# Performance work log

Measured on AMD Instinct MI355X. Metric: run time of the kernel, lower is better.

The kernel has to match this reference:

```python
import jax, jax.numpy as jnp
import numpy as np

D_MODEL = 768
N_HEAD = 12
D_K = D_MODEL // N_HEAD  # 64, also d_v
B, S = 2, 2048


def setup_inputs() -> dict:
    key = jax.random.key(0)
    ks = jax.random.split(key, 8)
    scale = 1.0 / np.sqrt(D_MODEL)
    return {
        "q": jax.random.normal(ks[0], (B, S, D_MODEL), dtype=jnp.float32),
        "k": jax.random.normal(ks[1], (B, S, D_MODEL), dtype=jnp.float32),
        "v": jax.random.normal(ks[2], (B, S, D_MODEL), dtype=jnp.float32),
        "mask": jax.random.randint(ks[3], (B, 1, S, S), 0, 2, dtype=jnp.int32),
        # per-head projection weights, stacked over heads: [H, d_model, d_k]
        "Wq": jax.random.normal(ks[4], (N_HEAD, D_MODEL, D_K), dtype=jnp.float32) * scale,
        "Wk": jax.random.normal(ks[5], (N_HEAD, D_MODEL, D_K), dtype=jnp.float32) * scale,
        "Wv": jax.random.normal(ks[6], (N_HEAD, D_MODEL, D_K), dtype=jnp.float32) * scale,
        # output projection: [n_head*d_v, d_model]
        "Wo": jax.random.normal(ks[7], (N_HEAD * D_K, D_MODEL), dtype=jnp.float32) * scale,
    }


def reference(q, k, v, mask, Wq, Wk, Wv, Wo):
    # Per-head projections (batched over heads instead of a python loop)
    qh = jnp.einsum("bsd,hdk->bhsk", q, Wq)  # [B,H,S,d_k]
    kh = jnp.einsum("bsd,hdk->bhsk", k, Wk)
    vh = jnp.einsum("bsd,hdk->bhsk", v, Wv)
    # Scaled dot-product attention with full score matrix (faithful to source)
    scores = jnp.einsum("bhsk,bhtk->bhst", qh, kh) / jnp.sqrt(jnp.asarray(D_K, qh.dtype))
    scores = jnp.where(mask == 0, jnp.asarray(-1e9, scores.dtype), scores)
    attn = jax.nn.softmax(scores, axis=-1)  # [B,H,S,S]
    out = jnp.einsum("bhst,bhtk->bhsk", attn, vh)  # [B,H,S,d_k]
    # concat heads (matches torch.cat over head outputs along last dim)
    out = out.transpose(0, 2, 1, 3).reshape(out.shape[0], out.shape[2], -1)  # [B,S,H*d_k]
    return out @ Wo  # [B,S,d_model]
```

## Files before the change

kernel.cpp:

```cpp
#include <hip/hip_runtime.h>
#include <stdint.h>

#define S_LEN 2048
#define NH 12
#define DM 768
#define DK 64
#define NB 2
#define MROWS (NB * S_LEN)

typedef __attribute__((ext_vector_type(8))) short short8;
typedef __attribute__((ext_vector_type(4))) float f32x4;
typedef __attribute__((ext_vector_type(4))) uint32_t u32x4;

__device__ __forceinline__ unsigned short bf16rne(float f) {
    union { float f; uint32_t u; } v; v.f = f;
    return (unsigned short)((v.u + 0x7FFFu + ((v.u >> 16) & 1u)) >> 16);
}

__device__ __forceinline__ uint32_t cvtpk(float lo, float hi) {
    uint32_t r;
    asm("v_cvt_pk_bf16_f32 %0, %1, %2" : "=v"(r) : "v"(lo), "v"(hi));
    return r;
}

__global__ __launch_bounds__(256) void prep_kernel(
        const float* __restrict__ Wq, const float* __restrict__ Wk,
        const float* __restrict__ Wv, const float* __restrict__ Wo,
        const int* __restrict__ mask,
        unsigned short* __restrict__ WqT, unsigned short* __restrict__ WkT,
        unsigned short* __restrict__ WvT, unsigned short* __restrict__ WoT,
        uint32_t* __restrict__ pm) {
    int bx = blockIdx.x;
    if (bx < 9216) {
        int which = bx / 2304;
        const float* W = (which == 0) ? Wq : (which == 1) ? Wk : (which == 2) ? Wv : Wo;
        unsigned short* WT = (which == 0) ? WqT : (which == 1) ? WkT : (which == 2) ? WvT : WoT;
        int idx = (bx % 2304) * 256 + threadIdx.x;
        int n = idx / DM, kd = idx % DM;
        float val;
        if (which < 3) { int h = n >> 6, kk = n & 63; val = W[(h * DM + kd) * DK + kk]; }
        else          { val = W[kd * DM + n]; }
        WT[idx] = bf16rne(val);
    } else {
        int t = (bx - 9216) * 256 + threadIdx.x;
        const int4* mp = (const int4*)mask;
        int4 a = mp[2 * t], b = mp[2 * t + 1];
        unsigned int by =
            (a.x != 0 ? 1u : 0u)  | (a.y != 0 ? 2u : 0u)  | (a.z != 0 ? 4u : 0u)  | (a.w != 0 ? 8u : 0u) |
            (b.x != 0 ? 16u : 0u) | (b.y != 0 ? 32u : 0u) | (b.z != 0 ? 64u : 0u) | (b.w != 0 ? 128u : 0u);
        ((unsigned char*)pm)[t] = (unsigned char)by;
    }
}

__device__ __forceinline__ void gemm_core(const unsigned short* __restrict__ A,
                                          const unsigned short* __restrict__ BT,
                                          unsigned short* As, unsigned short* Bs,
                                          f32x4 (&acc)[4][4]) {
    const int tid = threadIdx.x;
    const int lane = tid & 63, wid = tid >> 6;
    const int ww = wid & 1, wh = wid >> 1;
    const int quad = lane >> 4, l16 = lane & 15;
    const int lr = lane >> 2;
    const int lc = (lane & 3) * 8;
    typedef __attribute__((address_space(1))) const unsigned int* gp1;
    typedef __attribute__((address_space(3))) unsigned int* lp3;
    const unsigned short* Ag = A + (size_t)(wid * 32 + lr) * DM + lc;
    const unsigned short* Bg = BT + (size_t)(wid * 32 + lr) * DM + lc;
    unsigned short* Al = &As[wid * 32 * 32];
    unsigned short* Bl = &Bs[wid * 32 * 32];
    for (int kt = 0; kt < DM; kt += 32) {
        __syncthreads();
        __builtin_amdgcn_global_load_lds((gp1)(const void*)(Ag + kt),            (lp3)(void*)Al,             16, 0, 0);
        __builtin_amdgcn_global_load_lds((gp1)(const void*)(Ag + 16 * DM + kt),  (lp3)(void*)(Al + 16 * 32), 16, 0, 0);
        __builtin_amdgcn_global_load_lds((gp1)(const void*)(Bg + kt),            (lp3)(void*)Bl,             16, 0, 0);
        __builtin_amdgcn_global_load_lds((gp1)(const void*)(Bg + 16 * DM + kt),  (lp3)(void*)(Bl + 16 * 32), 16, 0, 0);
        __syncthreads();
        short8 af[4], bf[4];
#pragma unroll
        for (int i = 0; i < 4; ++i) af[i] = *(const short8*)&As[(wh * 64 + i * 16 + l16) * 32 + quad * 8];
#pragma unroll
        for (int j = 0; j < 4; ++j) bf[j] = *(const short8*)&Bs[(ww * 64 + j * 16 + l16) * 32 + quad * 8];
#pragma unroll
        for (int i = 0; i < 4; ++i)
#pragma unroll
            for (int j = 0; j < 4; ++j)
                acc[i][j] = __builtin_amdgcn_mfma_f32_16x16x32_bf16(af[i], bf[j], acc[i][j], 0, 0, 0);
    }
}

__device__ __forceinline__ void gemm_core_f32A(const float* __restrict__ A,
                                               const unsigned short* __restrict__ BT,
                                               unsigned short* As, unsigned short* Bs,
                                               f32x4 (&acc)[4][4]) {
    const int tid = threadIdx.x;
    const int lane = tid & 63, wid = tid >> 6;
    const int ww = wid & 1, wh = wid >> 1;
    const int quad = lane >> 4, l16 = lane & 15;
    const int lr = lane >> 2;
    const int lc = (lane & 3) * 8;
    typedef __attribute__((address_space(1))) const unsigned int* gp1;
    typedef __attribute__((address_space(3))) unsigned int* lp3;
    const float* Ag0 = A + (size_t)(wid * 32 + lr) * DM + lc;
    const float* Ag1 = A + (size_t)(wid * 32 + 16 + lr) * DM + lc;
    const unsigned short* Bg = BT + (size_t)(wid * 32 + lr) * DM + lc;
    unsigned short* Al = &As[wid * 32 * 32];
    unsigned short* Bl = &Bs[wid * 32 * 32];
    for (int kt = 0; kt < DM; kt += 32) {
        __syncthreads();
        __builtin_amdgcn_global_load_lds((gp1)(const void*)(Bg + kt),            (lp3)(void*)Bl,             16, 0, 0);
        __builtin_amdgcn_global_load_lds((gp1)(const void*)(Bg + 16 * DM + kt),  (lp3)(void*)(Bl + 16 * 32), 16, 0, 0);
        float4 x0 = *(const float4*)(Ag0 + kt), x1 = *(const float4*)(Ag0 + kt + 4);
        float4 y0 = *(const float4*)(Ag1 + kt), y1 = *(const float4*)(Ag1 + kt + 4);
        u32x4 ua, ub;
        ua[0] = cvtpk(x0.x, x0.y); ua[1] = cvtpk(x0.z, x0.w);
        ua[2] = cvtpk(x1.x, x1.y); ua[3] = cvtpk(x1.z, x1.w);
        ub[0] = cvtpk(y0.x, y0.y); ub[1] = cvtpk(y0.z, y0.w);
        ub[2] = cvtpk(y1.x, y1.y); ub[3] = cvtpk(y1.z, y1.w);
        *(u32x4*)&Al[lr * 32 + lc] = ua;
        *(u32x4*)&Al[(16 + lr) * 32 + lc] = ub;
        __syncthreads();
        short8 af[4], bf[4];
#pragma unroll
        for (int i = 0; i < 4; ++i) af[i] = *(const short8*)&As[(wh * 64 + i * 16 + l16) * 32 + quad * 8];
#pragma unroll
        for (int j = 0; j < 4; ++j) bf[j] = *(const short8*)&Bs[(ww * 64 + j * 16 + l16) * 32 + quad * 8];
#pragma unroll
        for (int i = 0; i < 4; ++i)
#pragma unroll
            for (int j = 0; j < 4; ++j)
                acc[i][j] = __builtin_amdgcn_mfma_f32_16x16x32_bf16(af[i], bf[j], acc[i][j], 0, 0, 0);
    }
}

__global__ __launch_bounds__(256) void proj_gemm(
        const float* __restrict__ qf32, const float* __restrict__ kf32,
        const float* __restrict__ vf32,
        const unsigned short* __restrict__ WqT, const unsigned short* __restrict__ WkT,
        const unsigned short* __restrict__ WvT,
        unsigned short* __restrict__ qh, unsigned short* __restrict__ kh,
        unsigned short* __restrict__ vhT) {
    __shared__ __align__(16) unsigned short As[128 * 32];
    __shared__ __align__(16) unsigned short Bs[128 * 32];
    const int z = blockIdx.z;
    const float* A = (z == 0) ? qf32 : (z == 1) ? kf32 : vf32;
    const unsigned short* BT = (z == 0) ? WqT : (z == 1) ? WkT : WvT;
    f32x4 acc[4][4] = {};
    gemm_core_f32A(A + (size_t)blockIdx.x * 128 * DM, BT + (size_t)blockIdx.y * 128 * DM, As, Bs, acc);

    const int tid = threadIdx.x;
    const int lane = tid & 63, wid = tid >> 6;
    const int ww = wid & 1, wh = wid >> 1;
    const int quad = lane >> 4, l16 = lane & 15;
    const int row0 = blockIdx.x * 128 + wh * 64;
    const int col0 = blockIdx.y * 128 + ww * 64;
    if (z < 2) {
        unsigned short* C = z ? kh : qh;
#pragma unroll
        for (int i = 0; i < 4; ++i)
#pragma unroll
            for (int j = 0; j < 4; ++j)
#pragma unroll
                for (int r = 0; r < 4; ++r)
                    C[(size_t)(row0 + i * 16 + quad * 4 + r) * DM + col0 + j * 16 + l16] = bf16rne(acc[i][j][r]);
    } else {
#pragma unroll
        for (int i = 0; i < 4; ++i)
#pragma unroll
            for (int j = 0; j < 4; ++j) {
                int row = row0 + i * 16 + quad * 4;
                int col = col0 + j * 16 + l16;
                int bb = row >> 11, s = row & 2047;
                int hh = col >> 6, d = col & 63;
                int g = (s >> 2) & 15;
                int pg = (g & 8) | ((g & 3) << 1) | ((g & 4) >> 2);
                int sp = (s & ~63) | (pg << 2) | (s & 3);
                uint32_t lo = (uint32_t)bf16rne(acc[i][j][0]) | ((uint32_t)bf16rne(acc[i][j][1]) << 16);
                uint32_t hi = (uint32_t)bf16rne(acc[i][j][2]) | ((uint32_t)bf16rne(acc[i][j][3]) << 16);
                uint2 o = make_uint2(lo, hi);
                *(uint2*)&vhT[(size_t)((bb * NH + hh) * DK + d) * S_LEN + sp] = o;
            }
    }
}

__global__ __launch_bounds__(256) void attn_kernel(
        const unsigned short* __restrict__ qh, const unsigned short* __restrict__ kh,
        const unsigned short* __restrict__ vhT, const uint32_t* __restrict__ pm,
        unsigned short* __restrict__ pob, float* __restrict__ lsb) {
    const int qt = blockIdx.x, h = blockIdx.y;
    const int b = blockIdx.z >> 1, ks = blockIdx.z & 1;
    const int tid = threadIdx.x, w = tid >> 6, lane = tid & 63;
    const int quad = lane >> 4, l16 = lane & 15;
    __shared__ __align__(16) unsigned short SMEM[2 * 64 * 64];
    unsigned short* Ks = SMEM;
    unsigned short* Vs = SMEM + 64 * 64;

    const int qrow0 = qt * 128 + w * 32;
    short8 qf[2][2];
#pragma unroll
    for (int mi = 0; mi < 2; ++mi) {
        const size_t qbase = (size_t)(b * S_LEN + qrow0 + mi * 16 + l16) * DM + h * DK;
        qf[mi][0] = *(const short8*)&qh[qbase + quad * 8];
        qf[mi][1] = *(const short8*)&qh[qbase + 32 + quad * 8];
    }
    short8 of = {};
    if (l16 == 0) {
#pragma unroll
        for (int j = 0; j < 8; ++j) of[j] = (short)0x3F80;
    }

    f32x4 out_t[2][4] = {};
    f32x4 outl[2] = {};

    const int srow = tid >> 2, scol = (tid & 3) << 4;
    const int ssw = (srow & 7) << 3;
    const int sc0 = srow * 64 + (scol ^ ssw);
    const int sc1 = srow * 64 + ((scol + 8) ^ ssw);
    const unsigned short* Kg = kh + (size_t)b * S_LEN * DM + h * DK;
    const unsigned short* Vg = vhT + (size_t)((b * NH + h) * DK) * S_LEN;
    const float SCL = 0.18033688011112042f;
    const float FM = 12.0f;
    const int kt0 = ks * (S_LEN / 2);

    short8 kr0, kr1, vr0, vr1;
    kr0 = *(const short8*)&Kg[(size_t)(kt0 + srow) * DM + scol];
    kr1 = *(const short8*)&Kg[(size_t)(kt0 + srow) * DM + scol + 8];
    vr0 = *(const short8*)&Vg[(size_t)srow * S_LEN + kt0 + scol];
    vr1 = *(const short8*)&Vg[(size_t)srow * S_LEN + kt0 + scol + 8];

    for (int kt = kt0; kt < kt0 + S_LEN / 2; kt += 64) {
        __syncthreads();
        *(short8*)&Ks[sc0] = kr0;
        *(short8*)&Ks[sc1] = kr1;
        *(short8*)&Vs[sc0] = vr0;
        *(short8*)&Vs[sc1] = vr1;
        __syncthreads();
        {
            const int kn = kt + 64;
            kr0 = *(const short8*)&Kg[(size_t)(kn + srow) * DM + scol];
            kr1 = *(const short8*)&Kg[(size_t)(kn + srow) * DM + scol + 8];
            vr0 = *(const short8*)&Vg[(size_t)srow * S_LEN + kn + scol];
            vr1 = *(const short8*)&Vg[(size_t)srow * S_LEN + kn + scol + 8];
        }
        uint2 mw[2];
#pragma unroll
        for (int mi = 0; mi < 2; ++mi)
            mw[mi] = *(const uint2*)&pm[(size_t)(b * S_LEN + qrow0 + mi * 16 + l16) * 64 + (kt >> 5)];

        u32x4 pf32[2][2];
#pragma unroll
        for (int cb = 0; cb < 4; ++cb) {
            const int krw = cb * 16 + l16, ksw = (krw & 7) << 3;
            short8 kf0 = *(const short8*)&Ks[krw * 64 + ((quad * 8) ^ ksw)];
            short8 kf1 = *(const short8*)&Ks[krw * 64 + ((32 + quad * 8) ^ ksw)];
#pragma unroll
            for (int mi = 0; mi < 2; ++mi) {
                f32x4 zz = {0.f, 0.f, 0.f, 0.f};
                zz = __builtin_amdgcn_mfma_f32_16x16x32_bf16(kf0, qf[mi][0], zz, 0, 0, 0);
                zz = __builtin_amdgcn_mfma_f32_16x16x32_bf16(kf1, qf[mi][1], zz, 0, 0, 0);
                uint32_t mword = (cb & 2) ? mw[mi].y : mw[mi].x;
                float e[4];
#pragma unroll
                for (int r = 0; r < 4; ++r) {
                    float ev = __builtin_amdgcn_exp2f(fmaf(zz[r], SCL, -FM));
                    int32_t mneg = __builtin_amdgcn_sbfe((int32_t)mword, ((cb & 1) << 4) + quad * 4 + r, 1);
                    e[r] = __uint_as_float(__float_as_uint(ev) & (uint32_t)mneg);
                }
                pf32[mi][cb >> 1][(cb & 1) * 2 + 0] = cvtpk(e[0], e[1]);
                pf32[mi][cb >> 1][(cb & 1) * 2 + 1] = cvtpk(e[2], e[3]);
            }
        }
        short8 pf[2][2];
#pragma unroll
        for (int mi = 0; mi < 2; ++mi) {
            pf[mi][0] = __builtin_bit_cast(short8, pf32[mi][0]);
            pf[mi][1] = __builtin_bit_cast(short8, pf32[mi][1]);
        }

        __builtin_amdgcn_s_setprio(1);
#pragma unroll
        for (int c2 = 0; c2 < 4; ++c2) {
            const int vrw = c2 * 16 + l16, vsw = (vrw & 7) << 3;
            short8 vf0 = *(const short8*)&Vs[vrw * 64 + ((quad * 8) ^ vsw)];
            short8 vf1 = *(const short8*)&Vs[vrw * 64 + ((32 + quad * 8) ^ vsw)];
#pragma unroll
            for (int mi = 0; mi < 2; ++mi) {
                out_t[mi][c2] = __builtin_amdgcn_mfma_f32_16x16x32_bf16(vf0, pf[mi][0], out_t[mi][c2], 0, 0, 0);
                out_t[mi][c2] = __builtin_amdgcn_mfma_f32_16x16x32_bf16(vf1, pf[mi][1], out_t[mi][c2], 0, 0, 0);
            }
        }
#pragma unroll
        for (int mi = 0; mi < 2; ++mi) {
            outl[mi] = __builtin_amdgcn_mfma_f32_16x16x32_bf16(of, pf[mi][0], outl[mi], 0, 0, 0);
            outl[mi] = __builtin_amdgcn_mfma_f32_16x16x32_bf16(of, pf[mi][1], outl[mi], 0, 0, 0);
        }
        __builtin_amdgcn_s_setprio(0);
    }

    const int pz = b * 2 + ks;
    if (quad == 0) {
#pragma unroll
        for (int mi = 0; mi < 2; ++mi)
            lsb[((size_t)pz * NH + h) * S_LEN + qrow0 + mi * 16 + l16] = outl[mi][0];
    }

    __syncthreads();
    unsigned short* Os = SMEM + w * 2048;
#pragma unroll
    for (int mi = 0; mi < 2; ++mi) {
        const int orow = mi * 16 + l16, osw = (orow & 7) << 3;
#pragma unroll
        for (int c2 = 0; c2 < 4; ++c2) {
            uint2 pw2;
            pw2.x = cvtpk(out_t[mi][c2][0], out_t[mi][c2][1]);
            pw2.y = cvtpk(out_t[mi][c2][2], out_t[mi][c2][3]);
            *(uint2*)&Os[orow * 64 + ((c2 * 16 + quad * 4) ^ osw)] = pw2;
        }
    }
    const int ql = lane >> 1, hf = lane & 1;
    const int qsw = (ql & 7) << 3;
    const int qg = qrow0 + ql;
    const size_t orowg = ((size_t)pz * S_LEN + qg) * DM + h * DK + hf * 32;
#pragma unroll
    for (int k2 = 0; k2 < 4; ++k2)
        *(short8*)&pob[orowg + k2 * 8] = *(const short8*)&Os[ql * 64 + ((hf * 32 + k2 * 8) ^ qsw)];
}

__global__ __launch_bounds__(256) void merge_kernel(const unsigned short* __restrict__ pob,
                                                    const float* __restrict__ lsb,
                                                    unsigned short* __restrict__ ao) {
    int t = blockIdx.x * 256 + threadIdx.x;
    int sg = t / 192;
    int c = (t - sg * 192) * 4;
    int b = sg >> 11, s = sg & 2047, h = c >> 6;
    float l = lsb[((size_t)(b * 2) * NH + h) * S_LEN + s] +
              lsb[((size_t)(b * 2 + 1) * NH + h) * S_LEN + s];
    float rl = 1.f / fmaxf(l, 1e-37f);
    uint2 a0 = *(const uint2*)&pob[((size_t)(b * 2) * S_LEN + s) * DM + c];
    uint2 a1 = *(const uint2*)&pob[((size_t)(b * 2 + 1) * S_LEN + s) * DM + c];
    float f0 = __uint_as_float((a0.x & 0xFFFFu) << 16) + __uint_as_float((a1.x & 0xFFFFu) << 16);
    float f1 = __uint_as_float((a0.x >> 16) << 16)     + __uint_as_float((a1.x >> 16) << 16);
    float f2 = __uint_as_float((a0.y & 0xFFFFu) << 16) + __uint_as_float((a1.y & 0xFFFFu) << 16);
    float f3 = __uint_as_float((a0.y >> 16) << 16)     + __uint_as_float((a1.y >> 16) << 16);
    uint32_t lo = (uint32_t)bf16rne(f0 * rl) | ((uint32_t)bf16rne(f1 * rl) << 16);
    uint32_t hi = (uint32_t)bf16rne(f2 * rl) | ((uint32_t)bf16rne(f3 * rl) << 16);
    uint2 o = make_uint2(lo, hi);
    *(uint2*)&ao[(size_t)sg * DM + c] = o;
}

__global__ __launch_bounds__(256) void out_gemm(const unsigned short* __restrict__ ao,
                                                const unsigned short* __restrict__ WoT,
                                                float* __restrict__ C) {
    __shared__ __align__(16) unsigned short As[128 * 32];
    __shared__ __align__(16) unsigned short Bs[128 * 32];
    f32x4 acc[4][4] = {};
    gemm_core(ao + (size_t)blockIdx.x * 128 * DM, WoT + (size_t)blockIdx.y * 128 * DM, As, Bs, acc);
    const int tid = threadIdx.x;
    const int lane = tid & 63, wid = tid >> 6;
    const int ww = wid & 1, wh = wid >> 1;
    const int quad = lane >> 4, l16 = lane & 15;
    const int row0 = blockIdx.x * 128 + wh * 64;
    const int col0 = blockIdx.y * 128 + ww * 64;
#pragma unroll
    for (int i = 0; i < 4; ++i)
#pragma unroll
        for (int j = 0; j < 4; ++j)
#pragma unroll
            for (int r = 0; r < 4; ++r)
                C[(size_t)(row0 + i * 16 + quad * 4 + r) * DM + col0 + j * 16 + l16] = acc[i][j][r];
}

extern "C" void kernel_launch(void* const* d_in, const int* in_sizes, int n_in,
                              void* d_out, int out_size, void* d_ws, size_t ws_size,
                              hipStream_t stream) {
    const float* q = (const float*)d_in[0];
    const float* k = (const float*)d_in[1];
    const float* v = (const float*)d_in[2];
    const int* mask = (const int*)d_in[3];
    const float* Wq = (const float*)d_in[4];
    const float* Wk = (const float*)d_in[5];
    const float* Wv = (const float*)d_in[6];
    const float* Wo = (const float*)d_in[7];
    float* out = (float*)d_out;

    char* ws = (char*)d_ws;
    size_t off = 0;
    auto alloc = [&](size_t bytes) {
        void* p = ws + off;
        off += (bytes + 255) & ~(size_t)255;
        return p;
    };
    const size_t MAT = (size_t)MROWS * DM * 2;
    const size_t WMAT = (size_t)DM * DM * 2;
    unsigned short* WqT = (unsigned short*)alloc(WMAT);
    unsigned short* WkT = (unsigned short*)alloc(WMAT);
    unsigned short* WvT = (unsigned short*)alloc(WMAT);
    unsigned short* WoT = (unsigned short*)alloc(WMAT);
    unsigned short* qh  = (unsigned short*)alloc(MAT);
    unsigned short* kh  = (unsigned short*)alloc(MAT);
    unsigned short* vhT = (unsigned short*)alloc(MAT);
    unsigned short* ao  = (unsigned short*)alloc(MAT);
    uint32_t* pmask     = (uint32_t*)alloc((size_t)NB * S_LEN * 64 * 4);
    unsigned short* pob = (unsigned short*)alloc((size_t)4 * S_LEN * DM * 2);
    float* lsb          = (float*)alloc((size_t)4 * NH * S_LEN * 4);

    prep_kernel<<<dim3(9216 + 4096), 256, 0, stream>>>(Wq, Wk, Wv, Wo, mask,
                                                       WqT, WkT, WvT, WoT, pmask);
    proj_gemm<<<dim3(32, 6, 3), 256, 0, stream>>>(q, k, v, WqT, WkT, WvT, qh, kh, vhT);
    attn_kernel<<<dim3(16, 12, 4), 256, 0, stream>>>(qh, kh, vhT, pmask, pob, lsb);
    merge_kernel<<<dim3(3072), 256, 0, stream>>>(pob, lsb, ao);
    out_gemm<<<dim3(32, 6), 256, 0, stream>>>(ao, WoT, out);
}
```

Baseline: 231.6 us.

## Fuse split-K merge into output GEMM, split attention 4-way with XCD mapping

Removes the separate merge kernel by having the output projection GEMM sum the four partial attention outputs, normalise them by the summed denominators, and write bf16 tiles into LDS on the fly. Attention now splits the key range into four chunks on a 1D grid remapped across XCDs, doubling the block count. The softmax scale is folded into the Q projection weights and the fixed exponent offset is removed, saving an FMA per score at some risk of exp overflow. Workspace is reused by aliasing the partial-output buffer onto the projection weight buffers.

```diff
diff --git a/kernel.cpp b/kernel.cpp
--- a/kernel.cpp
+++ b/kernel.cpp
@@ -40,6 +40,7 @@
         float val;
         if (which < 3) { int h = n >> 6, kk = n & 63; val = W[(h * DM + kd) * DK + kk]; }
         else          { val = W[kd * DM + n]; }
+        if (which == 0) val *= 0.18033688011112042f;
         WT[idx] = bf16rne(val);
     } else {
         int t = (bx - 9216) * 256 + threadIdx.x;
@@ -49,42 +50,6 @@
             (a.x != 0 ? 1u : 0u)  | (a.y != 0 ? 2u : 0u)  | (a.z != 0 ? 4u : 0u)  | (a.w != 0 ? 8u : 0u) |
             (b.x != 0 ? 16u : 0u) | (b.y != 0 ? 32u : 0u) | (b.z != 0 ? 64u : 0u) | (b.w != 0 ? 128u : 0u);
         ((unsigned char*)pm)[t] = (unsigned char)by;
-    }
-}
-
-__device__ __forceinline__ void gemm_core(const unsigned short* __restrict__ A,
-                                          const unsigned short* __restrict__ BT,
-                                          unsigned short* As, unsigned short* Bs,
-                                          f32x4 (&acc)[4][4]) {
-    const int tid = threadIdx.x;
-    const int lane = tid & 63, wid = tid >> 6;
-    const int ww = wid & 1, wh = wid >> 1;
-    const int quad = lane >> 4, l16 = lane & 15;
-    const int lr = lane >> 2;
-    const int lc = (lane & 3) * 8;
-    typedef __attribute__((address_space(1))) const unsigned int* gp1;
-    typedef __attribute__((address_space(3))) unsigned int* lp3;
-    const unsigned short* Ag = A + (size_t)(wid * 32 + lr) * DM + lc;
-    const unsigned short* Bg = BT + (size_t)(wid * 32 + lr) * DM + lc;
-    unsigned short* Al = &As[wid * 32 * 32];
-    unsigned short* Bl = &Bs[wid * 32 * 32];
-    for (int kt = 0; kt < DM; kt += 32) {
-        __syncthreads();
-        __builtin_amdgcn_global_load_lds((gp1)(const void*)(Ag + kt),            (lp3)(void*)Al,             16, 0, 0);
-        __builtin_amdgcn_global_load_lds((gp1)(const void*)(Ag + 16 * DM + kt),  (lp3)(void*)(Al + 16 * 32), 16, 0, 0);
-        __builtin_amdgcn_global_load_lds((gp1)(const void*)(Bg + kt),            (lp3)(void*)Bl,             16, 0, 0);
-        __builtin_amdgcn_global_load_lds((gp1)(const void*)(Bg + 16 * DM + kt),  (lp3)(void*)(Bl + 16 * 32), 16, 0, 0);
-        __syncthreads();
-        short8 af[4], bf[4];
-#pragma unroll
-        for (int i = 0; i < 4; ++i) af[i] = *(const short8*)&As[(wh * 64 + i * 16 + l16) * 32 + quad * 8];
-#pragma unroll
-        for (int j = 0; j < 4; ++j) bf[j] = *(const short8*)&Bs[(ww * 64 + j * 16 + l16) * 32 + quad * 8];
-#pragma unroll
-        for (int i = 0; i < 4; ++i)
-#pragma unroll
-            for (int j = 0; j < 4; ++j)
-                acc[i][j] = __builtin_amdgcn_mfma_f32_16x16x32_bf16(af[i], bf[j], acc[i][j], 0, 0, 0);
     }
 }
 
@@ -186,8 +151,14 @@
         const unsigned short* __restrict__ qh, const unsigned short* __restrict__ kh,
         const unsigned short* __restrict__ vhT, const uint32_t* __restrict__ pm,
         unsigned short* __restrict__ pob, float* __restrict__ lsb) {
-    const int qt = blockIdx.x, h = blockIdx.y;
-    const int b = blockIdx.z >> 1, ks = blockIdx.z & 1;
+    const int bid = blockIdx.x;
+    const int xcd = bid & 7, pos = bid >> 3;
+    const int wkr = xcd * 192 + pos;
+    const int qt = wkr & 15;
+    const int hz = wkr >> 4;
+    const int h = hz % 12;
+    const int z = hz / 12;
+    const int b = z >> 2, ks = z & 3;
     const int tid = threadIdx.x, w = tid >> 6, lane = tid & 63;
     const int quad = lane >> 4, l16 = lane & 15;
     __shared__ __align__(16) unsigned short SMEM[2 * 64 * 64];
@@ -217,9 +188,7 @@
     const int sc1 = srow * 64 + ((scol + 8) ^ ssw);
     const unsigned short* Kg = kh + (size_t)b * S_LEN * DM + h * DK;
     const unsigned short* Vg = vhT + (size_t)((b * NH + h) * DK) * S_LEN;
-    const float SCL = 0.18033688011112042f;
-    const float FM = 12.0f;
-    const int kt0 = ks * (S_LEN / 2);
+    const int kt0 = ks * (S_LEN / 4);
 
     short8 kr0, kr1, vr0, vr1;
     kr0 = *(const short8*)&Kg[(size_t)(kt0 + srow) * DM + scol];
@@ -227,7 +196,7 @@
     vr0 = *(const short8*)&Vg[(size_t)srow * S_LEN + kt0 + scol];
     vr1 = *(const short8*)&Vg[(size_t)srow * S_LEN + kt0 + scol + 8];
 
-    for (int kt = kt0; kt < kt0 + S_LEN / 2; kt += 64) {
+    for (int kt = kt0; kt < kt0 + S_LEN / 4; kt += 64) {
         __syncthreads();
         *(short8*)&Ks[sc0] = kr0;
         *(short8*)&Ks[sc1] = kr1;
@@ -261,7 +230,7 @@
                 float e[4];
 #pragma unroll
                 for (int r = 0; r < 4; ++r) {
-                    float ev = __builtin_amdgcn_exp2f(fmaf(zz[r], SCL, -FM));
+                    float ev = __builtin_amdgcn_exp2f(zz[r]);
                     int32_t mneg = __builtin_amdgcn_sbfe((int32_t)mword, ((cb & 1) << 4) + quad * 4 + r, 1);
                     e[r] = __uint_as_float(__float_as_uint(ev) & (uint32_t)mneg);
                 }
@@ -296,7 +265,7 @@
         __builtin_amdgcn_s_setprio(0);
     }
 
-    const int pz = b * 2 + ks;
+    const int pz = z;
     if (quad == 0) {
 #pragma unroll
         for (int mi = 0; mi < 2; ++mi)
@@ -325,39 +294,81 @@
         *(short8*)&pob[orowg + k2 * 8] = *(const short8*)&Os[ql * 64 + ((hf * 32 + k2 * 8) ^ qsw)];
 }
 
-__global__ __launch_bounds__(256) void merge_kernel(const unsigned short* __restrict__ pob,
-                                                    const float* __restrict__ lsb,
-                                                    unsigned short* __restrict__ ao) {
-    int t = blockIdx.x * 256 + threadIdx.x;
-    int sg = t / 192;
-    int c = (t - sg * 192) * 4;
-    int b = sg >> 11, s = sg & 2047, h = c >> 6;
-    float l = lsb[((size_t)(b * 2) * NH + h) * S_LEN + s] +
-              lsb[((size_t)(b * 2 + 1) * NH + h) * S_LEN + s];
-    float rl = 1.f / fmaxf(l, 1e-37f);
-    uint2 a0 = *(const uint2*)&pob[((size_t)(b * 2) * S_LEN + s) * DM + c];
-    uint2 a1 = *(const uint2*)&pob[((size_t)(b * 2 + 1) * S_LEN + s) * DM + c];
-    float f0 = __uint_as_float((a0.x & 0xFFFFu) << 16) + __uint_as_float((a1.x & 0xFFFFu) << 16);
-    float f1 = __uint_as_float((a0.x >> 16) << 16)     + __uint_as_float((a1.x >> 16) << 16);
-    float f2 = __uint_as_float((a0.y & 0xFFFFu) << 16) + __uint_as_float((a1.y & 0xFFFFu) << 16);
-    float f3 = __uint_as_float((a0.y >> 16) << 16)     + __uint_as_float((a1.y >> 16) << 16);
-    uint32_t lo = (uint32_t)bf16rne(f0 * rl) | ((uint32_t)bf16rne(f1 * rl) << 16);
-    uint32_t hi = (uint32_t)bf16rne(f2 * rl) | ((uint32_t)bf16rne(f3 * rl) << 16);
-    uint2 o = make_uint2(lo, hi);
-    *(uint2*)&ao[(size_t)sg * DM + c] = o;
-}
-
-__global__ __launch_bounds__(256) void out_gemm(const unsigned short* __restrict__ ao,
-                                                const unsigned short* __restrict__ WoT,
-                                                float* __restrict__ C) {
+__global__ __launch_bounds__(256) void out_gemm(
+        const unsigned short* __restrict__ pob, const float* __restrict__ lsb,
+        const unsigned short* __restrict__ WoT, float* __restrict__ C) {
     __shared__ __align__(16) unsigned short As[128 * 32];
     __shared__ __align__(16) unsigned short Bs[128 * 32];
-    f32x4 acc[4][4] = {};
-    gemm_core(ao + (size_t)blockIdx.x * 128 * DM, WoT + (size_t)blockIdx.y * 128 * DM, As, Bs, acc);
     const int tid = threadIdx.x;
     const int lane = tid & 63, wid = tid >> 6;
     const int ww = wid & 1, wh = wid >> 1;
     const int quad = lane >> 4, l16 = lane & 15;
+    const int lr = lane >> 2, lc = (lane & 3) * 8;
+    typedef __attribute__((address_space(1))) const unsigned int* gp1;
+    typedef __attribute__((address_space(3))) unsigned int* lp3;
+    const int ra0 = blockIdx.x * 128 + wid * 32 + lr;
+    const int ra1 = ra0 + 16;
+    const int bb = blockIdx.x >> 4;
+    const unsigned short* Bg = WoT + (size_t)(blockIdx.y * 128 + wid * 32 + lr) * DM + lc;
+    unsigned short* Al = &As[wid * 32 * 32];
+    unsigned short* Bl = &Bs[wid * 32 * 32];
+    size_t oa0[4], oa1[4];
+    int ol0[4], ol1[4];
+#pragma unroll
+    for (int ksp = 0; ksp < 4; ++ksp) {
+        int pz = bb * 4 + ksp;
+        oa0[ksp] = ((size_t)pz * S_LEN + (ra0 & 2047)) * DM + lc;
+        oa1[ksp] = ((size_t)pz * S_LEN + (ra1 & 2047)) * DM + lc;
+        ol0[ksp] = (pz * NH) * S_LEN + (ra0 & 2047);
+        ol1[ksp] = (pz * NH) * S_LEN + (ra1 & 2047);
+    }
+    f32x4 acc[4][4] = {};
+    for (int kt = 0; kt < DM; kt += 32) {
+        __syncthreads();
+        __builtin_amdgcn_global_load_lds((gp1)(const void*)(Bg + kt),           (lp3)(void*)Bl,            16, 0, 0);
+        __builtin_amdgcn_global_load_lds((gp1)(const void*)(Bg + 16 * DM + kt), (lp3)(void*)(Bl + 16 * 32), 16, 0, 0);
+        const int hh = kt >> 6;
+        float l0 = 0.f, l1 = 0.f;
+        short8 p0[4], p1[4];
+#pragma unroll
+        for (int ksp = 0; ksp < 4; ++ksp) {
+            p0[ksp] = *(const short8*)&pob[oa0[ksp] + kt];
+            p1[ksp] = *(const short8*)&pob[oa1[ksp] + kt];
+            l0 += lsb[ol0[ksp] + hh * S_LEN];
+            l1 += lsb[ol1[ksp] + hh * S_LEN];
+        }
+        float rl0 = 1.f / fmaxf(l0, 1e-37f);
+        float rl1 = 1.f / fmaxf(l1, 1e-37f);
+        u32x4 ua, ub;
+#pragma unroll
+        for (int e = 0; e < 4; ++e) {
+            float f0lo = 0.f, f0hi = 0.f, f1lo = 0.f, f1hi = 0.f;
+#pragma unroll
+            for (int ksp = 0; ksp < 4; ++ksp) {
+                uint32_t w0 = ((const u32x4&)p0[ksp])[e];
+                uint32_t w1 = ((const u32x4&)p1[ksp])[e];
+                f0lo += __uint_as_float(w0 << 16);
+                f0hi += __uint_as_float(w0 & 0xFFFF0000u);
+                f1lo += __uint_as_float(w1 << 16);
+                f1hi += __uint_as_float(w1 & 0xFFFF0000u);
+            }
+            ua[e] = cvtpk(f0lo * rl0, f0hi * rl0);
+            ub[e] = cvtpk(f1lo * rl1, f1hi * rl1);
+        }
+        *(u32x4*)&Al[lr * 32 + lc] = ua;
+        *(u32x4*)&Al[(16 + lr) * 32 + lc] = ub;
+        __syncthreads();
+        short8 af[4], bf[4];
+#pragma unroll
+        for (int i = 0; i < 4; ++i) af[i] = *(const short8*)&As[(wh * 64 + i * 16 + l16) * 32 + quad * 8];
+#pragma unroll
+        for (int j = 0; j < 4; ++j) bf[j] = *(const short8*)&Bs[(ww * 64 + j * 16 + l16) * 32 + quad * 8];
+#pragma unroll
+        for (int i = 0; i < 4; ++i)
+#pragma unroll
+            for (int j = 0; j < 4; ++j)
+                acc[i][j] = __builtin_amdgcn_mfma_f32_16x16x32_bf16(af[i], bf[j], acc[i][j], 0, 0, 0);
+    }
     const int row0 = blockIdx.x * 128 + wh * 64;
     const int col0 = blockIdx.y * 128 + ww * 64;
 #pragma unroll
@@ -391,22 +402,21 @@
     };
     const size_t MAT = (size_t)MROWS * DM * 2;
     const size_t WMAT = (size_t)DM * DM * 2;
-    unsigned short* WqT = (unsigned short*)alloc(WMAT);
-    unsigned short* WkT = (unsigned short*)alloc(WMAT);
-    unsigned short* WvT = (unsigned short*)alloc(WMAT);
     unsigned short* WoT = (unsigned short*)alloc(WMAT);
     unsigned short* qh  = (unsigned short*)alloc(MAT);
     unsigned short* kh  = (unsigned short*)alloc(MAT);
     unsigned short* vhT = (unsigned short*)alloc(MAT);
-    unsigned short* ao  = (unsigned short*)alloc(MAT);
     uint32_t* pmask     = (uint32_t*)alloc((size_t)NB * S_LEN * 64 * 4);
-    unsigned short* pob = (unsigned short*)alloc((size_t)4 * S_LEN * DM * 2);
-    float* lsb          = (float*)alloc((size_t)4 * NH * S_LEN * 4);
+    float* lsb          = (float*)alloc((size_t)8 * NH * S_LEN * 4);
+    unsigned short* WqT = (unsigned short*)alloc(WMAT);
+    unsigned short* WkT = (unsigned short*)alloc(WMAT);
+    unsigned short* WvT = (unsigned short*)alloc(WMAT);
+    unsigned short* pob = WqT;
+    (void)alloc((size_t)8 * S_LEN * DM * 2 - 3 * WMAT);
 
     prep_kernel<<<dim3(9216 + 4096), 256, 0, stream>>>(Wq, Wk, Wv, Wo, mask,
                                                        WqT, WkT, WvT, WoT, pmask);
     proj_gemm<<<dim3(32, 6, 3), 256, 0, stream>>>(q, k, v, WqT, WkT, WvT, qh, kh, vhT);
-    attn_kernel<<<dim3(16, 12, 4), 256, 0, stream>>>(qh, kh, vhT, pmask, pob, lsb);
-    merge_kernel<<<dim3(3072), 256, 0, stream>>>(pob, lsb, ao);
-    out_gemm<<<dim3(32, 6), 256, 0, stream>>>(ao, WoT, out);
-}
+    attn_kernel<<<dim3(1536), 256, 0, stream>>>(qh, kh, vhT, pmask, pob, lsb);
+    out_gemm<<<dim3(32, 6), 256, 0, stream>>>(pob, lsb, WoT, out);
+}
```

After: 239.4 us. 3.4% more time.
